# Kernel optimization log

Hardware: AMD Instinct MI355X
Metric: run time of the kernel (lower is better)

The kernel has to match this reference:

```python
import jax, jax.numpy as jnp
import numpy as np

B, G, F = 256, 2048, 128   # batch, graph_size, feat_size (== gcn_dim == k)
RNN_DIM = 512
K = F  # self.k = args.gcn_dim


def setup_inputs() -> dict:
    key = jax.random.key(0)
    k1, k2, k3 = jax.random.split(key, 3)
    node_embs = jax.random.normal(k1, (B, G, F), dtype=jnp.float32)
    mask = jnp.zeros((B, G), dtype=jnp.float32)
    h_t = jax.random.normal(k2, (B, RNN_DIM), dtype=jnp.float32)
    W_map = jax.random.normal(k3, (RNN_DIM, F), dtype=jnp.float32) * (1.0 / np.sqrt(RNN_DIM))
    b_map = jnp.zeros((F,), dtype=jnp.float32)
    return {"node_embs": node_embs, "mask": mask, "h_t": h_t, "W_map": W_map, "b_map": b_map}


def reference(node_embs, mask, h_t, W_map, b_map):
    # mapper: Linear + Tanh -> scorer [B, F]
    scorer = jnp.tanh(h_t @ W_map + b_map)
    # scores = bmm(node_embs, scorer) / ||scorer||  -> [B, G]
    norm = jnp.linalg.norm(scorer, axis=1, keepdims=True)  # [B, 1]
    scores = jnp.einsum('bgf,bf->bg', node_embs, scorer) / norm
    scores = scores + mask
    # top-k over graph dim (mask is all-zero so no -inf filtering/padding needed)
    vals, topk_indices = jax.lax.top_k(scores, K)  # [B, K]
    # gather node embeddings at topk indices, scale by tanh of gathered scores
    gathered = jnp.take_along_axis(node_embs, topk_indices[:, :, None], axis=1)  # [B, K, F]
    out = gathered * jnp.tanh(vals)[:, :, None]  # tanh(scores.gather) == tanh(vals)
    # log-softmax over graph dim, gather at topk, mean -> policy score [B]
    log_probs = jax.nn.log_softmax(scores, axis=-1)
    score = jnp.take_along_axis(log_probs, topk_indices, axis=-1)  # [B, K]
    policy_score = score.mean(axis=1)
    return (jnp.transpose(out, (0, 2, 1)), policy_score)  # ([B, F, K], [B])
```

## Files before the change

### kernel.cpp

```cpp
#include <hip/hip_runtime.h>
#include <cmath>

#define B_ 256
#define G_ 2048
#define F_ 128
#define RNN_ 512
#define K_ 128

__global__ __launch_bounds__(512) void k_scorer(const float* __restrict__ h_t,
                                                const float* __restrict__ W,
                                                const float* __restrict__ b_map,
                                                float* __restrict__ scorer_norm) {
    __shared__ float h[RNN_];
    __shared__ float part[4][F_];
    __shared__ float red8[8];
    const int b = blockIdx.x;
    const int tid = threadIdx.x;
    const int wv = tid >> 6;
    const int lane = tid & 63;
    h[tid] = h_t[b * RNN_ + tid];
    __syncthreads();
    {
        const int f = tid & 127;
        const int qu = tid >> 7;
        float acc = 0.f;
        const int r0 = qu * (RNN_ / 4);
#pragma unroll 8
        for (int r = r0; r < r0 + RNN_ / 4; ++r) acc += h[r] * W[r * F_ + f];
        part[qu][f] = acc;
    }
    __syncthreads();
    float tval = 0.f;
    if (tid < F_)
        tval = tanhf(part[0][tid] + part[1][tid] + part[2][tid] + part[3][tid] + b_map[tid]);
    float v = tval * tval;
#pragma unroll
    for (int off = 32; off; off >>= 1) v += __shfl_xor(v, off);
    if (lane == 0) red8[wv] = v;
    __syncthreads();
    if (tid == 0) {
        float s = 0.f;
#pragma unroll
        for (int i = 0; i < 8; ++i) s += red8[i];
        red8[0] = sqrtf(s);
    }
    __syncthreads();
    if (tid < F_) scorer_norm[b * F_ + tid] = tval / red8[0];
}

__global__ __launch_bounds__(256) void k_scores(const float* __restrict__ node,
                                                const float* __restrict__ mask,
                                                const float* __restrict__ scorer_norm,
                                                float* __restrict__ scores) {
    const int b = blockIdx.y;
    const int gbase = blockIdx.x * 64;
    const int tid = threadIdx.x;
    const int wave = tid >> 6;
    const int lane = tid & 63;
    const int half = lane >> 5;
    const int l32 = lane & 31;

    const float4 s4 = ((const float4*)(scorer_norm + b * F_))[l32];
    const float4* nb = (const float4*)(node + (size_t)b * G_ * F_);
    const int rowbase = gbase + wave * 16;
#pragma unroll
    for (int p = 0; p < 8; ++p) {
        const int g = rowbase + p * 2 + half;
        const float4 e = nb[(size_t)g * 32 + l32];
        float part = e.x * s4.x + e.y * s4.y + e.z * s4.z + e.w * s4.w;
        part += __shfl_xor(part, 16);
        part += __shfl_xor(part, 8);
        part += __shfl_xor(part, 4);
        part += __shfl_xor(part, 2);
        part += __shfl_xor(part, 1);
        if (l32 == 0) scores[b * G_ + g] = part + mask[b * G_ + g];
    }
}

__global__ __launch_bounds__(512) void k_selgather(const float* __restrict__ scores,
                                                   const float* __restrict__ node,
                                                   float* __restrict__ out,
                                                   float* __restrict__ policy) {
    __shared__ float sc[G_];
    __shared__ unsigned hist[2][8][256];
    __shared__ unsigned long long win[K_];
    __shared__ float tile[K_][33];
    __shared__ float valk[K_];
    __shared__ float tanhv[K_];
    __shared__ int idxk[K_];
    __shared__ float red8[8];
    __shared__ unsigned long long prefix_sh;
    __shared__ int need_sh;
    __shared__ int done_sh;
    __shared__ int cnt;

    const int b = blockIdx.x;
    const int tid = threadIdx.x;
    const int wv = tid >> 6;
    const int lane = tid & 63;

    for (int i = tid; i < 8 * 256; i += 512) ((unsigned*)hist[0])[i] = 0u;
    if (tid == 0) { cnt = 0; done_sh = 0; }

    unsigned long long kreg[4];
    {
        const float4 v4 = ((const float4*)(scores + b * G_))[tid];
        const float vv[4] = {v4.x, v4.y, v4.z, v4.w};
#pragma unroll
        for (int p = 0; p < 4; ++p) {
            const int i = tid * 4 + p;
            sc[i] = vv[p];
            unsigned u = __float_as_uint(vv[p]);
            u = (u & 0x80000000u) ? ~u : (u | 0x80000000u);
            kreg[p] = ((unsigned long long)u << 32) | (unsigned)(G_ - 1 - i);
        }
    }
    __syncthreads();

    unsigned long long prefix = 0ull;
    int need = K_;
    int round = 0;
    for (int shift = 56; shift >= 0; shift -= 8, ++round) {
        unsigned(*H)[256] = hist[round & 1];
        const unsigned long long hi_mask = (shift == 56) ? 0ull : (~0ull << (shift + 8));
#pragma unroll
        for (int p = 0; p < 4; ++p) {
            const unsigned long long key = kreg[p];
            if ((key & hi_mask) == prefix)
                atomicAdd(&H[wv][(unsigned)(key >> shift) & 255u], 1u);
        }
        __syncthreads();
        if (wv == 0) {
            const int L = lane;
            unsigned h0 = 0, h1 = 0, h2 = 0, h3 = 0;
#pragma unroll
            for (int ww = 0; ww < 8; ++ww) {
                h0 += H[ww][4 * L + 0];
                h1 += H[ww][4 * L + 1];
                h2 += H[ww][4 * L + 2];
                h3 += H[ww][4 * L + 3];
            }
            const unsigned s3 = h3, s2 = h2 + s3, s1 = h1 + s2, s0 = h0 + s1;
            unsigned S = s0;
            for (int off = 1; off < 64; off <<= 1) {
                const unsigned tt = __shfl_down(S, off);
                if (L + off < 64) S += tt;
            }
            unsigned Snext = __shfl_down(S, 1);
            if (L == 63) Snext = 0;
            const unsigned un = (unsigned)need;
            const unsigned suf0 = Snext + s0, suf1 = Snext + s1;
            const unsigned suf2 = Snext + s2, suf3 = Snext + s3, suf4 = Snext;
            int d = -1;
            unsigned sd = 0, sd1 = 0;
            if (suf0 >= un && suf1 < un) { d = 4 * L + 0; sd = suf0; sd1 = suf1; }
            else if (suf1 >= un && suf2 < un) { d = 4 * L + 1; sd = suf1; sd1 = suf2; }
            else if (suf2 >= un && suf3 < un) { d = 4 * L + 2; sd = suf2; sd1 = suf3; }
            else if (suf3 >= un && suf4 < un) { d = 4 * L + 3; sd = suf3; sd1 = suf4; }
            if (d >= 0) {
                prefix_sh = prefix | ((unsigned long long)(unsigned)d << shift);
                need_sh = need - (int)sd1;
                done_sh = (sd == un);
            }
        } else {
            unsigned* Z = (unsigned*)hist[(round + 1) & 1];
            for (int i = tid - 64; i < 8 * 256; i += 448) Z[i] = 0u;
        }
        __syncthreads();
        prefix = prefix_sh;
        need = need_sh;
        if (done_sh) break;
    }
    const unsigned long long T = prefix;

#pragma unroll
    for (int p = 0; p < 4; ++p) {
        if (kreg[p] >= T) {
            const int q = atomicAdd(&cnt, 1);
            if (q < K_) win[q] = kreg[p];
        }
    }
    __syncthreads();

    if (tid < K_) {
        const unsigned long long mykey = win[tid];
        int rank = 0;
#pragma unroll 8
        for (int j = 0; j < K_; ++j) rank += (win[j] > mykey) ? 1 : 0;
        const int idx = G_ - 1 - (int)(unsigned)(mykey & 0xFFFFFFFFull);
        const float val = sc[idx];
        idxk[rank] = idx;
        valk[rank] = val;
        tanhv[rank] = tanhf(val);
    }
    __syncthreads();

    const float maxv = valk[0];
    float s = 0.f;
#pragma unroll
    for (int p = 0; p < 4; ++p) s += expf(sc[tid + p * 512] - maxv);
#pragma unroll
    for (int off = 32; off; off >>= 1) s += __shfl_xor(s, off);
    if (lane == 0) red8[wv] = s;
    __syncthreads();
    if (tid == 0) {
        float tot = 0.f;
#pragma unroll
        for (int i = 0; i < 8; ++i) tot += red8[i];
        const float lse = maxv + logf(tot);
        float sum = 0.f;
        for (int k = 0; k < K_; ++k) sum += valk[k];
        policy[b] = sum * (1.0f / K_) - lse;
    }

    const float* nbase = node + (size_t)b * G_ * F_;
    float* ob = out + (size_t)b * F_ * K_;
    for (int f0 = 0; f0 < F_; f0 += 32) {
        for (int e = tid; e < K_ * 8; e += 512) {
            const int k2 = e >> 3;
            const int q = e & 7;
            const float4 vv = *(const float4*)(nbase + (size_t)idxk[k2] * F_ + f0 + 4 * q);
            tile[k2][4 * q + 0] = vv.x;
            tile[k2][4 * q + 1] = vv.y;
            tile[k2][4 * q + 2] = vv.z;
            tile[k2][4 * q + 3] = vv.w;
        }
        __syncthreads();
        for (int e = tid; e < 32 * K_; e += 512) {
            const int f = e >> 7;
            const int k2 = e & 127;
            ob[(size_t)(f0 + f) * K_ + k2] = tile[k2][f] * tanhv[k2];
        }
        __syncthreads();
    }
}

extern "C" void kernel_launch(void* const* d_in, const int* in_sizes, int n_in,
                              void* d_out, int out_size, void* d_ws, size_t ws_size,
                              hipStream_t stream) {
    const float* node = (const float*)d_in[0];
    const float* mask = (const float*)d_in[1];
    const float* h_t = (const float*)d_in[2];
    const float* W = (const float*)d_in[3];
    const float* bm = (const float*)d_in[4];

    float* out = (float*)d_out;
    float* policy = out + (size_t)B_ * F_ * K_;

    float* scorer_norm = (float*)d_ws;
    float* scores = scorer_norm + B_ * F_;

    k_scorer<<<B_, 512, 0, stream>>>(h_t, W, bm, scorer_norm);
    k_scores<<<dim3(G_ / 64, B_), 256, 0, stream>>>(node, mask, scorer_norm, scores);
    k_selgather<<<B_, 512, 0, stream>>>(scores, node, out, policy);
}
```

Before: 388.9 us.

## Fuse scorer, score computation and top-k gather into one kernel per batch

Merges the three kernels into a single 1024-thread block per batch row: the scorer vector is computed in shared memory, the node-by-scorer dot products are written straight into shared scores, and the radix top-k, log-softmax and gather follow in the same block. This removes two launches and the global round trip of the scores and scorer arrays. It also prefetches the next gather tile into registers while the current tile is being stored. In exchange the large node read now runs with only one block per batch, so memory-level parallelism for the bandwidth-heavy score pass depends on 16 waves per CU instead of thousands of small blocks.

```diff
diff --git a/kernel.cpp b/kernel.cpp
--- a/kernel.cpp
+++ b/kernel.cpp
@@ -7,127 +7,128 @@
 #define RNN_ 512
 #define K_ 128
 
-__global__ __launch_bounds__(512) void k_scorer(const float* __restrict__ h_t,
+__global__ __launch_bounds__(1024) void k_fused(const float* __restrict__ node,
+                                                const float* __restrict__ mask,
+                                                const float* __restrict__ h_t,
                                                 const float* __restrict__ W,
                                                 const float* __restrict__ b_map,
-                                                float* __restrict__ scorer_norm) {
-    __shared__ float h[RNN_];
-    __shared__ float part[4][F_];
-    __shared__ float red8[8];
+                                                float* __restrict__ out,
+                                                float* __restrict__ policy) {
+    __shared__ __align__(16) float sc[G_];
+    __shared__ unsigned hist[2][8][256];
+    __shared__ __align__(16) float tile[K_][33];
+    __shared__ __align__(16) float sn[F_];
+    __shared__ unsigned long long win[K_];
+    __shared__ float valk[K_];
+    __shared__ float tanhv[K_];
+    __shared__ int idxk[K_];
+    __shared__ float red16[16];
+    __shared__ unsigned long long prefix_sh;
+    __shared__ int need_sh;
+    __shared__ int done_sh;
+    __shared__ int cnt;
+
     const int b = blockIdx.x;
     const int tid = threadIdx.x;
     const int wv = tid >> 6;
     const int lane = tid & 63;
-    h[tid] = h_t[b * RNN_ + tid];
+
+    float* hsm = &tile[0][0];
+    float(*wp)[F_] = (float(*)[F_])(hsm + RNN_);
+    if (tid < RNN_) hsm[tid] = h_t[b * RNN_ + tid];
+    if (tid == 0) { cnt = 0; done_sh = 0; }
+    for (int i = tid; i < 8 * 256; i += 1024) ((unsigned*)hist[0])[i] = 0u;
     __syncthreads();
     {
         const int f = tid & 127;
         const int qu = tid >> 7;
         float acc = 0.f;
-        const int r0 = qu * (RNN_ / 4);
+        const int r0 = qu * (RNN_ / 8);
 #pragma unroll 8
-        for (int r = r0; r < r0 + RNN_ / 4; ++r) acc += h[r] * W[r * F_ + f];
-        part[qu][f] = acc;
+        for (int r = r0; r < r0 + RNN_ / 8; ++r) acc += hsm[r] * W[r * F_ + f];
+        wp[qu][f] = acc;
     }
     __syncthreads();
     float tval = 0.f;
-    if (tid < F_)
-        tval = tanhf(part[0][tid] + part[1][tid] + part[2][tid] + part[3][tid] + b_map[tid]);
+    if (tid < F_) {
+        float a = b_map[tid];
+#pragma unroll
+        for (int q = 0; q < 8; ++q) a += wp[q][tid];
+        tval = tanhf(a);
+    }
     float v = tval * tval;
 #pragma unroll
     for (int off = 32; off; off >>= 1) v += __shfl_xor(v, off);
-    if (lane == 0) red8[wv] = v;
-    __syncthreads();
-    if (tid == 0) {
-        float s = 0.f;
-#pragma unroll
-        for (int i = 0; i < 8; ++i) s += red8[i];
-        red8[0] = sqrtf(s);
-    }
-    __syncthreads();
-    if (tid < F_) scorer_norm[b * F_ + tid] = tval / red8[0];
-}
-
-__global__ __launch_bounds__(256) void k_scores(const float* __restrict__ node,
-                                                const float* __restrict__ mask,
-                                                const float* __restrict__ scorer_norm,
-                                                float* __restrict__ scores) {
-    const int b = blockIdx.y;
-    const int gbase = blockIdx.x * 64;
-    const int tid = threadIdx.x;
-    const int wave = tid >> 6;
-    const int lane = tid & 63;
-    const int half = lane >> 5;
-    const int l32 = lane & 31;
-
-    const float4 s4 = ((const float4*)(scorer_norm + b * F_))[l32];
-    const float4* nb = (const float4*)(node + (size_t)b * G_ * F_);
-    const int rowbase = gbase + wave * 16;
-#pragma unroll
-    for (int p = 0; p < 8; ++p) {
-        const int g = rowbase + p * 2 + half;
-        const float4 e = nb[(size_t)g * 32 + l32];
-        float part = e.x * s4.x + e.y * s4.y + e.z * s4.z + e.w * s4.w;
-        part += __shfl_xor(part, 16);
-        part += __shfl_xor(part, 8);
-        part += __shfl_xor(part, 4);
-        part += __shfl_xor(part, 2);
-        part += __shfl_xor(part, 1);
-        if (l32 == 0) scores[b * G_ + g] = part + mask[b * G_ + g];
-    }
-}
-
-__global__ __launch_bounds__(512) void k_selgather(const float* __restrict__ scores,
-                                                   const float* __restrict__ node,
-                                                   float* __restrict__ out,
-                                                   float* __restrict__ policy) {
-    __shared__ float sc[G_];
-    __shared__ unsigned hist[2][8][256];
-    __shared__ unsigned long long win[K_];
-    __shared__ float tile[K_][33];
-    __shared__ float valk[K_];
-    __shared__ float tanhv[K_];
-    __shared__ int idxk[K_];
-    __shared__ float red8[8];
-    __shared__ unsigned long long prefix_sh;
-    __shared__ int need_sh;
-    __shared__ int done_sh;
-    __shared__ int cnt;
-
-    const int b = blockIdx.x;
-    const int tid = threadIdx.x;
-    const int wv = tid >> 6;
-    const int lane = tid & 63;
-
-    for (int i = tid; i < 8 * 256; i += 512) ((unsigned*)hist[0])[i] = 0u;
-    if (tid == 0) { cnt = 0; done_sh = 0; }
-
-    unsigned long long kreg[4];
+    if (tid == 0) red16[0] = v;
+    if (tid == 64) red16[1] = v;
+    __syncthreads();
+    if (tid < F_) sn[tid] = tval / sqrtf(red16[0] + red16[1]);
+    __syncthreads();
+
     {
-        const float4 v4 = ((const float4*)(scores + b * G_))[tid];
-        const float vv[4] = {v4.x, v4.y, v4.z, v4.w};
-#pragma unroll
-        for (int p = 0; p < 4; ++p) {
-            const int i = tid * 4 + p;
-            sc[i] = vv[p];
-            unsigned u = __float_as_uint(vv[p]);
-            u = (u & 0x80000000u) ? ~u : (u | 0x80000000u);
-            kreg[p] = ((unsigned long long)u << 32) | (unsigned)(G_ - 1 - i);
-        }
+        const int hw = tid >> 5;
+        const int l32 = tid & 31;
+        const float4 s4 = ((const float4*)sn)[l32];
+        const float4* nb = (const float4*)(node + (size_t)b * (G_ * F_));
+#pragma unroll 2
+        for (int r = 0; r < 64; r += 4) {
+            const float4 e0 = nb[(size_t)(((r + 0) << 5) + hw) * 32 + l32];
+            const float4 e1 = nb[(size_t)(((r + 1) << 5) + hw) * 32 + l32];
+            const float4 e2 = nb[(size_t)(((r + 2) << 5) + hw) * 32 + l32];
+            const float4 e3 = nb[(size_t)(((r + 3) << 5) + hw) * 32 + l32];
+            float p0 = e0.x * s4.x + e0.y * s4.y + e0.z * s4.z + e0.w * s4.w;
+            float p1 = e1.x * s4.x + e1.y * s4.y + e1.z * s4.z + e1.w * s4.w;
+            float p2 = e2.x * s4.x + e2.y * s4.y + e2.z * s4.z + e2.w * s4.w;
+            float p3 = e3.x * s4.x + e3.y * s4.y + e3.z * s4.z + e3.w * s4.w;
+#pragma unroll
+            for (int off = 16; off; off >>= 1) {
+                p0 += __shfl_xor(p0, off);
+                p1 += __shfl_xor(p1, off);
+                p2 += __shfl_xor(p2, off);
+                p3 += __shfl_xor(p3, off);
+            }
+            if (l32 == 0) {
+                sc[((r + 0) << 5) + hw] = p0;
+                sc[((r + 1) << 5) + hw] = p1;
+                sc[((r + 2) << 5) + hw] = p2;
+                sc[((r + 3) << 5) + hw] = p3;
+            }
+        }
+    }
+    __syncthreads();
+
+    unsigned long long kreg[2];
+    float vv0, vv1;
+    {
+        const float2 v2 = ((const float2*)sc)[tid];
+        const float2 m2 = ((const float2*)(mask + (size_t)b * G_))[tid];
+        vv0 = v2.x + m2.x;
+        vv1 = v2.y + m2.y;
+        float2 wb;
+        wb.x = vv0;
+        wb.y = vv1;
+        ((float2*)sc)[tid] = wb;
+        unsigned u0 = __float_as_uint(vv0);
+        u0 = (u0 & 0x80000000u) ? ~u0 : (u0 | 0x80000000u);
+        kreg[0] = ((unsigned long long)u0 << 32) | (unsigned)(G_ - 1 - (2 * tid + 0));
+        unsigned u1 = __float_as_uint(vv1);
+        u1 = (u1 & 0x80000000u) ? ~u1 : (u1 | 0x80000000u);
+        kreg[1] = ((unsigned long long)u1 << 32) | (unsigned)(G_ - 1 - (2 * tid + 1));
     }
     __syncthreads();
 
     unsigned long long prefix = 0ull;
     int need = K_;
     int round = 0;
+    const int wv8 = wv & 7;
     for (int shift = 56; shift >= 0; shift -= 8, ++round) {
         unsigned(*H)[256] = hist[round & 1];
         const unsigned long long hi_mask = (shift == 56) ? 0ull : (~0ull << (shift + 8));
 #pragma unroll
-        for (int p = 0; p < 4; ++p) {
+        for (int p = 0; p < 2; ++p) {
             const unsigned long long key = kreg[p];
             if ((key & hi_mask) == prefix)
-                atomicAdd(&H[wv][(unsigned)(key >> shift) & 255u], 1u);
+                atomicAdd(&H[wv8][(unsigned)(key >> shift) & 255u], 1u);
         }
         __syncthreads();
         if (wv == 0) {
@@ -164,7 +165,7 @@
             }
         } else {
             unsigned* Z = (unsigned*)hist[(round + 1) & 1];
-            for (int i = tid - 64; i < 8 * 256; i += 448) Z[i] = 0u;
+            for (int i = tid - 64; i < 8 * 256; i += 1024 - 64) Z[i] = 0u;
         }
         __syncthreads();
         prefix = prefix_sh;
@@ -174,14 +175,13 @@
     const unsigned long long T = prefix;
 
 #pragma unroll
-    for (int p = 0; p < 4; ++p) {
+    for (int p = 0; p < 2; ++p) {
         if (kreg[p] >= T) {
             const int q = atomicAdd(&cnt, 1);
             if (q < K_) win[q] = kreg[p];
         }
     }
     __syncthreads();
-
     if (tid < K_) {
         const unsigned long long mykey = win[tid];
         int rank = 0;
@@ -196,40 +196,40 @@
     __syncthreads();
 
     const float maxv = valk[0];
-    float s = 0.f;
-#pragma unroll
-    for (int p = 0; p < 4; ++p) s += expf(sc[tid + p * 512] - maxv);
+    float s = expf(vv0 - maxv) + expf(vv1 - maxv);
 #pragma unroll
     for (int off = 32; off; off >>= 1) s += __shfl_xor(s, off);
-    if (lane == 0) red8[wv] = s;
+    if (lane == 0) red16[wv] = s;
     __syncthreads();
     if (tid == 0) {
         float tot = 0.f;
 #pragma unroll
-        for (int i = 0; i < 8; ++i) tot += red8[i];
+        for (int i = 0; i < 16; ++i) tot += red16[i];
         const float lse = maxv + logf(tot);
         float sum = 0.f;
         for (int k = 0; k < K_; ++k) sum += valk[k];
         policy[b] = sum * (1.0f / K_) - lse;
     }
 
-    const float* nbase = node + (size_t)b * G_ * F_;
-    float* ob = out + (size_t)b * F_ * K_;
+    const float* nbase = node + (size_t)b * (G_ * F_);
+    float* ob = out + (size_t)b * (F_ * K_);
+    const int k2 = tid >> 3;
+    const int q8 = tid & 7;
+    float4 pre = *(const float4*)(nbase + (size_t)idxk[k2] * F_ + 4 * q8);
     for (int f0 = 0; f0 < F_; f0 += 32) {
-        for (int e = tid; e < K_ * 8; e += 512) {
-            const int k2 = e >> 3;
-            const int q = e & 7;
-            const float4 vv = *(const float4*)(nbase + (size_t)idxk[k2] * F_ + f0 + 4 * q);
-            tile[k2][4 * q + 0] = vv.x;
-            tile[k2][4 * q + 1] = vv.y;
-            tile[k2][4 * q + 2] = vv.z;
-            tile[k2][4 * q + 3] = vv.w;
-        }
-        __syncthreads();
-        for (int e = tid; e < 32 * K_; e += 512) {
+        tile[k2][4 * q8 + 0] = pre.x;
+        tile[k2][4 * q8 + 1] = pre.y;
+        tile[k2][4 * q8 + 2] = pre.z;
+        tile[k2][4 * q8 + 3] = pre.w;
+        __syncthreads();
+        if (f0 + 32 < F_)
+            pre = *(const float4*)(nbase + (size_t)idxk[k2] * F_ + (f0 + 32) + 4 * q8);
+#pragma unroll
+        for (int j = 0; j < 4; ++j) {
+            const int e = tid + j * 1024;
             const int f = e >> 7;
-            const int k2 = e & 127;
-            ob[(size_t)(f0 + f) * K_ + k2] = tile[k2][f] * tanhv[k2];
+            const int kk = e & 127;
+            ob[(size_t)(f0 + f) * K_ + kk] = tile[kk][f] * tanhv[kk];
         }
         __syncthreads();
     }
@@ -247,10 +247,5 @@
     float* out = (float*)d_out;
     float* policy = out + (size_t)B_ * F_ * K_;
 
-    float* scorer_norm = (float*)d_ws;
-    float* scores = scorer_norm + B_ * F_;
-
-    k_scorer<<<B_, 512, 0, stream>>>(h_t, W, bm, scorer_norm);
-    k_scores<<<dim3(G_ / 64, B_), 256, 0, stream>>>(node, mask, scorer_norm, scores);
-    k_selgather<<<B_, 512, 0, stream>>>(scores, node, out, policy);
+    k_fused<<<B_, 1024, 0, stream>>>(node, mask, h_t, W, bm, out, policy);
 }
```

Measured after the change: 377.5 us. 1.03x faster.
